# Kernel tuning notes

Measured on AMD Instinct MI355X. Metric: run time of the kernel, lower is better.

## Reference

```python
import jax, jax.numpy as jnp
import numpy as np

B, L, D, H = 4, 2048, 1024, 16
HD = D // H
NEG = -1e9  # stands in for -inf in masks; identical softmax result, grad-safe
EPS = 1e-5


def _layer_norm(x, g, b):
    mu = jnp.mean(x, axis=-1, keepdims=True)
    var = jnp.mean((x - mu) ** 2, axis=-1, keepdims=True)
    return (x - mu) * jax.lax.rsqrt(var + EPS) * g + b


def setup_inputs() -> dict:
    key = jax.random.key(0)
    ks = jax.random.split(key, 8)
    x = jax.random.normal(ks[0], (B, L, D), dtype=jnp.float32)
    # length-based padding: valid lengths in [L//2, L]; True = padded position
    lengths = jax.random.randint(ks[1], (B,), L // 2, L + 1)
    padding_mask = jnp.arange(L)[None, :] >= lengths[:, None]  # (B, L) bool
    # additive causal mask: 0 on/below diagonal, NEG above
    causal_mask = jnp.where(jnp.tril(jnp.ones((L, L), dtype=bool)), 0.0, NEG).astype(jnp.float32)

    def linear_params(k, fan_in, fan_out):
        bound = float(np.sqrt(6.0 / (fan_in + fan_out)))  # xavier_uniform
        W = jax.random.uniform(k, (fan_out, fan_in), jnp.float32, -bound, bound)
        b = jnp.zeros((fan_out,), jnp.float32)
        return W, b

    Wq, bq = linear_params(ks[2], D, D)
    Wk, bk = linear_params(ks[3], D, D)
    Wv, bv = linear_params(ks[4], D, D)
    Wo, bo = linear_params(ks[5], D, D)
    g_pre = jnp.ones((D,), jnp.float32); b_pre = jnp.zeros((D,), jnp.float32)
    g_ln = jnp.ones((D,), jnp.float32); b_ln = jnp.zeros((D,), jnp.float32)
    return {
        "x": x, "padding_mask": padding_mask, "causal_mask": causal_mask,
        "Wq": Wq, "bq": bq, "Wk": Wk, "bk": bk, "Wv": Wv, "bv": bv,
        "Wo": Wo, "bo": bo, "g_pre": g_pre, "b_pre": b_pre,
        "g_ln": g_ln, "b_ln": b_ln,
    }


def reference(x, padding_mask, causal_mask, Wq, bq, Wk, bk, Wv, bv, Wo, bo,
              g_pre, b_pre, g_ln, b_ln):
    # pre-LayerNorm (residual uses the normed x, matching the torch code)
    h = _layer_norm(x, g_pre, b_pre)  # (B, L, D)

    def heads(W, b):
        y = jnp.einsum('bld,ed->ble', h, W) + b           # torch Linear: x @ W.T + b
        return y.reshape(B, L, H, HD).transpose(0, 2, 1, 3)  # (B, H, L, HD)

    q, k, v = heads(Wq, bq), heads(Wk, bk), heads(Wv, bv)

    scores = jnp.einsum('bhld,bhmd->bhlm', q, k) / jnp.sqrt(jnp.float32(HD))
    scores = scores + causal_mask  # additive causal mask broadcast over (B, H)
    # padding mask: True = masked key position
    scores = jnp.where(padding_mask[:, None, None, :], NEG, scores)
    attn = jax.nn.softmax(scores, axis=-1)  # dropout p=0.0 (eval / disabled)

    out = jnp.einsum('bhlm,bhmd->bhld', attn, v)          # (B, H, L, HD)
    out = out.transpose(0, 2, 1, 3).reshape(B, L, D)
    out = jnp.einsum('bld,ed->ble', out, Wo) + bo
    return _layer_norm(out + h, g_ln, b_ln)
```

## Files before the change

kernel.cpp:

```cpp
#include <hip/hip_runtime.h>


#define Bq 4
#define Lq 2048
#define Dq 1024
#define Hq 16
#define HDq 64
#define Mq (Bq * Lq)

typedef __attribute__((ext_vector_type(8))) short short8;
typedef __attribute__((ext_vector_type(4))) float f32x4;
typedef __attribute__((address_space(3))) unsigned char lds_byte;
typedef __attribute__((address_space(1))) unsigned char gbl_byte;

__device__ __forceinline__ unsigned short f2b(float f) {
    unsigned int u = __float_as_uint(f);
    unsigned int r = (u + 0x7fffu + ((u >> 16) & 1u)) >> 16;
    return (unsigned short)r;
}
__device__ __forceinline__ float b2f(unsigned short u) {
    return __uint_as_float(((unsigned int)u) << 16);
}
__device__ __forceinline__ unsigned int packbf(float lo, float hi) {
    return (unsigned int)f2b(lo) | ((unsigned int)f2b(hi) << 16);
}

#define GLL16(gsrc, ldst)                                              \
    __builtin_amdgcn_global_load_lds((const gbl_byte*)(gsrc),          \
                                     (lds_byte*)(ldst), 16, 0, 0)

__global__ void setup_kernel(const unsigned char* __restrict__ m8,
                             int* __restrict__ lengths) {
    __shared__ int bad;
    __shared__ int fo[4];
    const int tid = threadIdx.x;
    if (tid == 0) bad = 0;
    if (tid < 4) fo[tid] = Lq;
    __syncthreads();
    for (int i = tid; i < Bq * Lq; i += 256) {
        unsigned char v = m8[i];
        if (v) {
            int r = i >> 11, c = i & (Lq - 1);
            atomicMin(&fo[r], c);
            if (c < Lq / 2) atomicOr(&bad, 1);
            else if (c < Lq - 1 && m8[i + 1] == 0) atomicOr(&bad, 1);
        }
    }
    __syncthreads();
    int anyone = (fo[0] < Lq) | (fo[1] < Lq) | (fo[2] < Lq) | (fo[3] < Lq);
    bool use8 = (bad == 0) && anyone;
    if (!use8) {
        __syncthreads();
        if (tid < 4) fo[tid] = Lq;
        __syncthreads();
        const int* m32 = (const int*)m8;
        for (int i = tid; i < Bq * Lq; i += 256) {
            if (m32[i] != 0) atomicMin(&fo[i >> 11], i & (Lq - 1));
        }
        __syncthreads();
    }
    if (tid < 4) lengths[tid] = fo[tid];
}

__global__ __launch_bounds__(256) void cvt4_kernel(
    const float* __restrict__ s0, const float* __restrict__ s1,
    const float* __restrict__ s2, const float* __restrict__ s3,
    unsigned short* __restrict__ dst) {
    const int region = blockIdx.x >> 10;
    const int i = (blockIdx.x & 1023) * 256 + threadIdx.x;
    const float* src = (region == 0) ? s0 : (region == 1) ? s1
                       : (region == 2) ? s2 : s3;
    float4 v = ((const float4*)src)[i];
    ushort4 o;
    o.x = f2b(v.x); o.y = f2b(v.y); o.z = f2b(v.z); o.w = f2b(v.w);
    ((ushort4*)dst)[(size_t)region * (Dq * Dq / 4) + i] = o;
}

__global__ __launch_bounds__(256) void ln_pre_kernel(
    const float* __restrict__ x, const float* __restrict__ g,
    const float* __restrict__ bb, unsigned short* __restrict__ out) {
    const int row = blockIdx.x, tid = threadIdx.x;
    float4 u = ((const float4*)x)[(size_t)row * 256 + tid];
    float s = u.x + u.y + u.z + u.w;
    float ss = u.x * u.x + u.y * u.y + u.z * u.z + u.w * u.w;
#pragma unroll
    for (int off = 32; off > 0; off >>= 1) {
        s += __shfl_xor(s, off);
        ss += __shfl_xor(ss, off);
    }
    __shared__ float sred[4], ssred[4];
    const int w = tid >> 6, lane = tid & 63;
    if (lane == 0) { sred[w] = s; ssred[w] = ss; }
    __syncthreads();
    s = sred[0] + sred[1] + sred[2] + sred[3];
    ss = ssred[0] + ssred[1] + ssred[2] + ssred[3];
    const float mean = s * (1.f / Dq);
    const float rstd = rsqrtf(ss * (1.f / Dq) - mean * mean + 1e-5f);
    float4 gv = ((const float4*)g)[tid];
    float4 bv = ((const float4*)bb)[tid];
    ushort4 o;
    o.x = f2b((u.x - mean) * rstd * gv.x + bv.x);
    o.y = f2b((u.y - mean) * rstd * gv.y + bv.y);
    o.z = f2b((u.z - mean) * rstd * gv.z + bv.z);
    o.w = f2b((u.w - mean) * rstd * gv.w + bv.w);
    ((ushort4*)out)[(size_t)row * 256 + tid] = o;
}

__global__ __launch_bounds__(256) void qkv_gemm_kernel(
    const unsigned short* __restrict__ A, const unsigned short* __restrict__ W3,
    const float* __restrict__ bq, const float* __restrict__ bk,
    const float* __restrict__ bv, unsigned short* __restrict__ Qo,
    unsigned short* __restrict__ Ko, unsigned short* __restrict__ Vto) {
    __shared__ unsigned short As[128][32];
    __shared__ unsigned short Bs[128][32];
    const int tid = threadIdx.x;
    const int w = tid >> 6, lane = tid & 63;
    const int lm = lane & 15, lq = lane >> 4;
    const int m0 = blockIdx.y << 7, n0 = blockIdx.x << 7;
    const int wm = (w >> 1) << 6, wn = (w & 1) << 6;
    f32x4 acc[4][4];
#pragma unroll
    for (int i = 0; i < 4; ++i)
#pragma unroll
        for (int j = 0; j < 4; ++j) acc[i][j] = (f32x4){0.f, 0.f, 0.f, 0.f};
    for (int k0 = 0; k0 < Dq; k0 += 32) {
        __syncthreads();
#pragma unroll
        for (int j = 0; j < 2; ++j) {
            const int base = j * 256 + w * 64;
            const int slot = base + lane;
            const int row = slot >> 2, c = slot & 3;
            GLL16(A + (size_t)(m0 + row) * Dq + k0 + c * 8,
                  (unsigned short*)As + base * 8);
            GLL16(W3 + (size_t)(n0 + row) * Dq + k0 + c * 8,
                  (unsigned short*)Bs + base * 8);
        }
        __syncthreads();
        short8 af[4], bf[4];
#pragma unroll
        for (int t = 0; t < 4; ++t)
            af[t] = *(const short8*)&As[wm + t * 16 + lm][lq * 8];
#pragma unroll
        for (int t = 0; t < 4; ++t)
            bf[t] = *(const short8*)&Bs[wn + t * 16 + lm][lq * 8];
#pragma unroll
        for (int mt = 0; mt < 4; ++mt)
#pragma unroll
            for (int nt = 0; nt < 4; ++nt)
                acc[mt][nt] = __builtin_amdgcn_mfma_f32_16x16x32_bf16(
                    af[mt], bf[nt], acc[mt][nt], 0, 0, 0);
    }
    const int region = n0 >> 10;
    const float* bias = (region == 0) ? bq : (region == 1) ? bk : bv;
    const float scale = (region == 0) ? 0.125f : 1.0f;
    const int nb = n0 & 1023;
#pragma unroll
    for (int nt = 0; nt < 4; ++nt) {
        const int colb = nb + wn + nt * 16 + lm;
        const float bval = bias[colb];
#pragma unroll
        for (int mt = 0; mt < 4; ++mt) {
            const int row0 = m0 + wm + mt * 16 + lq * 4;
            const int bidx = row0 >> 11, l0r = row0 & (Lq - 1);
            if (region < 2) {
                unsigned short* dst = (region == 0) ? Qo : Ko;
#pragma unroll
                for (int r = 0; r < 4; ++r)
                    dst[((size_t)(bidx * Hq + (colb >> 6)) * Lq + l0r + r) *
                            HDq + (colb & 63)] =
                        f2b((acc[mt][nt][r] + bval) * scale);
            } else {
                ushort4 o;
                o.x = f2b(acc[mt][nt][0] + bval);
                o.y = f2b(acc[mt][nt][1] + bval);
                o.z = f2b(acc[mt][nt][2] + bval);
                o.w = f2b(acc[mt][nt][3] + bval);
                *(ushort4*)&Vto[((size_t)(bidx * Hq + (colb >> 6)) * HDq +
                                 (colb & 63)) * Lq + l0r] = o;
            }
        }
    }
}

__global__ __launch_bounds__(256) void proj_gemm_kernel(
    const unsigned short* __restrict__ A, const unsigned short* __restrict__ Bw,
    const float* __restrict__ bias, float* __restrict__ Cout) {
    __shared__ unsigned short As[128][32];
    __shared__ unsigned short Bs[128][32];
    const int tid = threadIdx.x;
    const int w = tid >> 6, lane = tid & 63;
    const int lm = lane & 15, lq = lane >> 4;
    const int m0 = blockIdx.y << 7, n0 = blockIdx.x << 7;
    const int wm = (w >> 1) << 6, wn = (w & 1) << 6;
    f32x4 acc[4][4];
#pragma unroll
    for (int i = 0; i < 4; ++i)
#pragma unroll
        for (int j = 0; j < 4; ++j) acc[i][j] = (f32x4){0.f, 0.f, 0.f, 0.f};
    for (int k0 = 0; k0 < Dq; k0 += 32) {
        __syncthreads();
#pragma unroll
        for (int j = 0; j < 2; ++j) {
            const int base = j * 256 + w * 64;
            const int slot = base + lane;
            const int row = slot >> 2, c = slot & 3;
            const int rr = m0 + row, kk = k0 + c * 8;
            GLL16(A + ((size_t)((rr >> 11) * Hq + (kk >> 6)) * Lq +
                       (rr & (Lq - 1))) * HDq + (kk & 63),
                  (unsigned short*)As + base * 8);
            GLL16(Bw + (size_t)(n0 + row) * Dq + k0 + c * 8,
                  (unsigned short*)Bs + base * 8);
        }
        __syncthreads();
        short8 af[4], bf[4];
#pragma unroll
        for (int t = 0; t < 4; ++t)
            af[t] = *(const short8*)&As[wm + t * 16 + lm][lq * 8];
#pragma unroll
        for (int t = 0; t < 4; ++t)
            bf[t] = *(const short8*)&Bs[wn + t * 16 + lm][lq * 8];
#pragma unroll
        for (int mt = 0; mt < 4; ++mt)
#pragma unroll
            for (int nt = 0; nt < 4; ++nt)
                acc[mt][nt] = __builtin_amdgcn_mfma_f32_16x16x32_bf16(
                    af[mt], bf[nt], acc[mt][nt], 0, 0, 0);
    }
#pragma unroll
    for (int nt = 0; nt < 4; ++nt) {
        const float bval = bias[n0 + wn + nt * 16 + lm];
#pragma unroll
        for (int mt = 0; mt < 4; ++mt)
#pragma unroll
            for (int r = 0; r < 4; ++r)
                Cout[(size_t)(m0 + wm + mt * 16 + lq * 4 + r) * Dq + n0 + wn +
                     nt * 16 + lm] = acc[mt][nt][r] + bval;
    }
}

__global__ __launch_bounds__(256) void attn_kernel(
    const unsigned short* __restrict__ Qg, const unsigned short* __restrict__ Kg,
    const unsigned short* __restrict__ Vtg, const int* __restrict__ lengths,
    unsigned short* __restrict__ Og) {
    __shared__ unsigned short Ps[4][16][72];
    const int bx = blockIdx.x;
    const int hh = blockIdx.y, b = blockIdx.z;
    const int tid = threadIdx.x, w = tid >> 6, lane = tid & 63;
    const int lm = lane & 15, lq = lane >> 4;
    const int len = lengths[b];
    const int mxk = (len + 63) >> 6;
    const size_t hb = (size_t)(b * Hq + hh) * Lq * HDq;
    const unsigned short* Vb = Vtg + hb;

#pragma unroll
    for (int pass = 0; pass < 2; ++pass) {
        const int qt = pass ? bx : (15 - bx);
        const int l0 = qt << 7;
        short8 qf[2][2];
#pragma unroll
        for (int s = 0; s < 2; ++s)
#pragma unroll
            for (int h = 0; h < 2; ++h)
                qf[s][h] = *(const short8*)(Qg + hb +
                    (size_t)(l0 + w * 32 + s * 16 + lm) * HDq + h * 32 + lq * 8);
        f32x4 oacc[2][4];
        float m_i[2], l_i[2];
#pragma unroll
        for (int s = 0; s < 2; ++s) {
            m_i[s] = -1e30f; l_i[s] = 0.f;
#pragma unroll
            for (int t = 0; t < 4; ++t)
                oacc[s][t] = (f32x4){0.f, 0.f, 0.f, 0.f};
        }
        int nkt = 2 * qt + 2;
        if (nkt > mxk) nkt = mxk;
        for (int kt = 0; kt < nkt; ++kt) {
            const int kb = kt << 6;
            short8 kf[4][2], vf[4][2];
#pragma unroll
            for (int t = 0; t < 4; ++t)
#pragma unroll
                for (int h = 0; h < 2; ++h)
                    kf[t][h] = *(const short8*)(Kg + hb +
                        (size_t)(kb + t * 16 + lm) * HDq + h * 32 + lq * 8);
#pragma unroll
            for (int t = 0; t < 4; ++t)
#pragma unroll
                for (int kh = 0; kh < 2; ++kh)
                    vf[t][kh] = *(const short8*)(Vb +
                        (size_t)(t * 16 + lm) * Lq + kb + kh * 32 + lq * 8);
#pragma unroll
            for (int s = 0; s < 2; ++s) {
                f32x4 sc[4];
#pragma unroll
                for (int t = 0; t < 4; ++t) {
                    f32x4 z = (f32x4){0.f, 0.f, 0.f, 0.f};
                    z = __builtin_amdgcn_mfma_f32_16x16x32_bf16(
                        kf[t][0], qf[s][0], z, 0, 0, 0);
                    z = __builtin_amdgcn_mfma_f32_16x16x32_bf16(
                        kf[t][1], qf[s][1], z, 0, 0, 0);
                    sc[t] = z;
                }
                const int qmin = l0 + w * 32 + s * 16;
                float pvv[16];
                float mx = -1e30f;
                if ((kb + 63 <= qmin) && (kb + 63 < len)) {
#pragma unroll
                    for (int i = 0; i < 16; ++i) {
                        const float v = sc[i >> 2][i & 3];
                        pvv[i] = v;
                        mx = fmaxf(mx, v);
                    }
                } else {
                    const int q = qmin + lm;
#pragma unroll
                    for (int t = 0; t < 4; ++t)
#pragma unroll
                        for (int r = 0; r < 4; ++r) {
                            const int key = kb + t * 16 + lq * 4 + r;
                            float v = sc[t][r];
                            if (key > q || key >= len) v = -1e30f;
                            pvv[t * 4 + r] = v;
                            mx = fmaxf(mx, v);
                        }
                }
                mx = fmaxf(mx, __shfl_xor(mx, 16));
                mx = fmaxf(mx, __shfl_xor(mx, 32));
                const float mnew = fmaxf(m_i[s], mx);
                const float alpha = __expf(m_i[s] - mnew);
                m_i[s] = mnew;
                float psum = 0.f;
#pragma unroll
                for (int i = 0; i < 16; ++i) {
                    const float p = __expf(pvv[i] - mnew);
                    pvv[i] = p;
                    psum += p;
                }
                psum += __shfl_xor(psum, 16);
                psum += __shfl_xor(psum, 32);
                l_i[s] = l_i[s] * alpha + psum;
#pragma unroll
                for (int t = 0; t < 4; ++t) {
                    oacc[s][t][0] *= alpha; oacc[s][t][1] *= alpha;
                    oacc[s][t][2] *= alpha; oacc[s][t][3] *= alpha;
                }
#pragma unroll
                for (int t = 0; t < 4; ++t) {
                    uint2 uu;
                    uu.x = packbf(pvv[t * 4 + 0], pvv[t * 4 + 1]);
                    uu.y = packbf(pvv[t * 4 + 2], pvv[t * 4 + 3]);
                    *(uint2*)&Ps[w][lm][t * 16 + lq * 4] = uu;
                }
                asm volatile("s_waitcnt lgkmcnt(0)" ::: "memory");
                short8 pf0 = *(const short8*)&Ps[w][lm][lq * 8];
                short8 pf1 = *(const short8*)&Ps[w][lm][32 + lq * 8];
#pragma unroll
                for (int t = 0; t < 4; ++t) {
                    oacc[s][t] = __builtin_amdgcn_mfma_f32_16x16x32_bf16(
                        vf[t][0], pf0, oacc[s][t], 0, 0, 0);
                    oacc[s][t] = __builtin_amdgcn_mfma_f32_16x16x32_bf16(
                        vf[t][1], pf1, oacc[s][t], 0, 0, 0);
                }
            }
        }
#pragma unroll
        for (int s = 0; s < 2; ++s) {
            const float inv = 1.f / l_i[s];
            unsigned short* Ot =
                Og + hb + (size_t)(l0 + w * 32 + s * 16 + lm) * HDq;
#pragma unroll
            for (int t = 0; t < 4; ++t) {
                ushort4 o;
                o.x = f2b(oacc[s][t][0] * inv);
                o.y = f2b(oacc[s][t][1] * inv);
                o.z = f2b(oacc[s][t][2] * inv);
                o.w = f2b(oacc[s][t][3] * inv);
                *(ushort4*)(Ot + t * 16 + lq * 4) = o;
            }
        }
    }
}

__global__ __launch_bounds__(256) void ln_final_kernel(
    const float* __restrict__ pj, const unsigned short* __restrict__ h,
    const float* __restrict__ g, const float* __restrict__ bb,
    float* __restrict__ out) {
    const int row = blockIdx.x, tid = threadIdx.x;
    float4 a = ((const float4*)pj)[(size_t)row * 256 + tid];
    ushort4 hv = ((const ushort4*)h)[(size_t)row * 256 + tid];
    float f0 = a.x + b2f(hv.x), f1 = a.y + b2f(hv.y);
    float f2 = a.z + b2f(hv.z), f3 = a.w + b2f(hv.w);
    float s = f0 + f1 + f2 + f3;
    float ss = f0 * f0 + f1 * f1 + f2 * f2 + f3 * f3;
#pragma unroll
    for (int off = 32; off > 0; off >>= 1) {
        s += __shfl_xor(s, off);
        ss += __shfl_xor(ss, off);
    }
    __shared__ float sred[4], ssred[4];
    const int w = tid >> 6, lane = tid & 63;
    if (lane == 0) { sred[w] = s; ssred[w] = ss; }
    __syncthreads();
    s = sred[0] + sred[1] + sred[2] + sred[3];
    ss = ssred[0] + ssred[1] + ssred[2] + ssred[3];
    const float mean = s * (1.f / Dq);
    const float rstd = rsqrtf(ss * (1.f / Dq) - mean * mean + 1e-5f);
    float4 gv = ((const float4*)g)[tid];
    float4 bv = ((const float4*)bb)[tid];
    float4 o;
    o.x = (f0 - mean) * rstd * gv.x + bv.x;
    o.y = (f1 - mean) * rstd * gv.y + bv.y;
    o.z = (f2 - mean) * rstd * gv.z + bv.z;
    o.w = (f3 - mean) * rstd * gv.w + bv.w;
    ((float4*)out)[(size_t)row * 256 + tid] = o;
}

extern "C" void kernel_launch(void* const* d_in, const int* in_sizes, int n_in,
                              void* d_out, int out_size, void* d_ws,
                              size_t ws_size, hipStream_t stream) {
    const float* x = (const float*)d_in[0];
    const unsigned char* mask = (const unsigned char*)d_in[1];
    const float* Wq = (const float*)d_in[3];
    const float* bq = (const float*)d_in[4];
    const float* Wk = (const float*)d_in[5];
    const float* bk = (const float*)d_in[6];
    const float* Wv = (const float*)d_in[7];
    const float* bvv = (const float*)d_in[8];
    const float* Wo = (const float*)d_in[9];
    const float* bo = (const float*)d_in[10];
    const float* g_pre = (const float*)d_in[11];
    const float* b_pre = (const float*)d_in[12];
    const float* g_ln = (const float*)d_in[13];
    const float* b_ln = (const float*)d_in[14];

    const size_t SZ = (size_t)Mq * Dq;
    const size_t WSZ = (size_t)Dq * Dq;
    unsigned short* h = (unsigned short*)d_ws;
    unsigned short* q = h + SZ;
    unsigned short* k = q + SZ;
    unsigned short* vT = k + SZ;
    unsigned short* at = vT + SZ;
    unsigned short* W3 = at + SZ;
    unsigned short* wob = W3 + 3 * WSZ;
    float* proj = (float*)(wob + WSZ);
    int* lengths = (int*)(proj + SZ);

    setup_kernel<<<1, 256, 0, stream>>>(mask, lengths);
    cvt4_kernel<<<4096, 256, 0, stream>>>(Wq, Wk, Wv, Wo, W3);
    ln_pre_kernel<<<Mq, 256, 0, stream>>>(x, g_pre, b_pre, h);

    qkv_gemm_kernel<<<dim3(3 * Dq / 128, Mq / 128), 256, 0, stream>>>(
        h, W3, bq, bk, bvv, q, k, vT);
    attn_kernel<<<dim3(Lq / 256, Hq, Bq), 256, 0, stream>>>(q, k, vT, lengths,
                                                            at);
    proj_gemm_kernel<<<dim3(Dq / 128, Mq / 128), 256, 0, stream>>>(at, wob, bo,
                                                                   proj);
    ln_final_kernel<<<Mq, 256, 0, stream>>>(proj, h, g_ln, b_ln,
                                            (float*)d_out);
}
```

Before: 408.6 us.

## Double-buffer K/V tiles in LDS for attention and swizzle GEMM block order

The attention kernel now stages K and V tiles into XOR-swizzled LDS double buffers with async global-to-LDS loads. The next tile is prefetched while the current one is computed, replacing per-wave direct global loads. It also splits the QK MFMA phase from the softmax/PV phase, adds s_setprio around MFMA bursts, and sets occupancy launch bounds. Separately, the QKV and output projection GEMMs remap block indices for better L2 locality. The cost is more LDS per block and one extra barrier per key tile.

```diff
diff --git a/kernel.cpp b/kernel.cpp
--- a/kernel.cpp
+++ b/kernel.cpp
@@ -28,6 +28,9 @@
 #define GLL16(gsrc, ldst)                                              \
     __builtin_amdgcn_global_load_lds((const gbl_byte*)(gsrc),          \
                                      (lds_byte*)(ldst), 16, 0, 0)
+
+#define MFMA_BF16(A, B, C) \
+    __builtin_amdgcn_mfma_f32_16x16x32_bf16((A), (B), (C), 0, 0, 0)
 
 __global__ void setup_kernel(const unsigned char* __restrict__ m8,
                              int* __restrict__ lengths) {
@@ -116,7 +119,9 @@
     const int tid = threadIdx.x;
     const int w = tid >> 6, lane = tid & 63;
     const int lm = lane & 15, lq = lane >> 4;
-    const int m0 = blockIdx.y << 7, n0 = blockIdx.x << 7;
+    const int lin = blockIdx.y * 24 + blockIdx.x;
+    const int swz = (lin & 7) * (1536 / 8) + (lin >> 3);
+    const int m0 = (swz / 24) << 7, n0 = (swz % 24) << 7;
     const int wm = (w >> 1) << 6, wn = (w & 1) << 6;
     f32x4 acc[4][4];
 #pragma unroll
@@ -190,7 +195,9 @@
     const int tid = threadIdx.x;
     const int w = tid >> 6, lane = tid & 63;
     const int lm = lane & 15, lq = lane >> 4;
-    const int m0 = blockIdx.y << 7, n0 = blockIdx.x << 7;
+    const int lin = blockIdx.y * 8 + blockIdx.x;
+    const int swz = (lin & 7) * (512 / 8) + (lin >> 3);
+    const int m0 = (swz >> 3) << 7, n0 = (swz & 7) << 7;
     const int wm = (w >> 1) << 6, wn = (w & 1) << 6;
     f32x4 acc[4][4];
 #pragma unroll
@@ -238,11 +245,13 @@
     }
 }
 
-__global__ __launch_bounds__(256) void attn_kernel(
+__global__ __launch_bounds__(256, 2) void attn_kernel(
     const unsigned short* __restrict__ Qg, const unsigned short* __restrict__ Kg,
     const unsigned short* __restrict__ Vtg, const int* __restrict__ lengths,
     unsigned short* __restrict__ Og) {
-    __shared__ unsigned short Ps[4][16][72];
+    __shared__ unsigned short Kbuf[2][4096];
+    __shared__ unsigned short Vbuf[2][4096];
+    __shared__ unsigned short Ps[4][2][16][72];
     const int bx = blockIdx.x;
     const int hh = blockIdx.y, b = blockIdx.z;
     const int tid = threadIdx.x, w = tid >> 6, lane = tid & 63;
@@ -252,6 +261,21 @@
     const size_t hb = (size_t)(b * Hq + hh) * Lq * HDq;
     const unsigned short* Vb = Vtg + hb;
 
+    const int srow = w * 8 + (lane >> 3);
+    const int ssw = (lane & 7) ^ (lane >> 3);
+    const unsigned short* pK = Kg + hb + (size_t)srow * HDq + ssw * 8;
+    const unsigned short* pV = Vb + (size_t)srow * Lq + ssw * 8;
+
+#define STAGE_KV(BUF, KB)                                                   \
+    {                                                                       \
+        GLL16(pK + (size_t)(KB)*HDq, &Kbuf[(BUF)][(w * 64) * 8]);           \
+        GLL16(pK + (size_t)((KB) + 32) * HDq,                               \
+              &Kbuf[(BUF)][(256 + w * 64) * 8]);                            \
+        GLL16(pV + (KB), &Vbuf[(BUF)][(w * 64) * 8]);                       \
+        GLL16(pV + (size_t)32 * Lq + (KB),                                  \
+              &Vbuf[(BUF)][(256 + w * 64) * 8]);                            \
+    }
+
 #pragma unroll
     for (int pass = 0; pass < 2; ++pass) {
         const int qt = pass ? bx : (15 - bx);
@@ -274,52 +298,58 @@
         }
         int nkt = 2 * qt + 2;
         if (nkt > mxk) nkt = mxk;
+        STAGE_KV(0, 0);
+        __syncthreads();
         for (int kt = 0; kt < nkt; ++kt) {
             const int kb = kt << 6;
+            const int cur = kt & 1;
+            if (kt + 1 < nkt) STAGE_KV(cur ^ 1, (kt + 1) << 6);
             short8 kf[4][2], vf[4][2];
 #pragma unroll
-            for (int t = 0; t < 4; ++t)
-#pragma unroll
-                for (int h = 0; h < 2; ++h)
-                    kf[t][h] = *(const short8*)(Kg + hb +
-                        (size_t)(kb + t * 16 + lm) * HDq + h * 32 + lq * 8);
-#pragma unroll
-            for (int t = 0; t < 4; ++t)
-#pragma unroll
-                for (int kh = 0; kh < 2; ++kh)
-                    vf[t][kh] = *(const short8*)(Vb +
-                        (size_t)(t * 16 + lm) * Lq + kb + kh * 32 + lq * 8);
+            for (int t = 0; t < 4; ++t) {
+                const int ro = (t * 16 + lm) * 64;
+                const int sx = lm & 7;
+#pragma unroll
+                for (int h = 0; h < 2; ++h) {
+                    const int off = ro + (((h * 4 + lq) ^ sx) << 3);
+                    kf[t][h] = *(const short8*)&Kbuf[cur][off];
+                    vf[t][h] = *(const short8*)&Vbuf[cur][off];
+                }
+            }
+            f32x4 sc[2][4];
+            __builtin_amdgcn_s_setprio(1);
 #pragma unroll
             for (int s = 0; s < 2; ++s) {
-                f32x4 sc[4];
 #pragma unroll
                 for (int t = 0; t < 4; ++t) {
                     f32x4 z = (f32x4){0.f, 0.f, 0.f, 0.f};
-                    z = __builtin_amdgcn_mfma_f32_16x16x32_bf16(
-                        kf[t][0], qf[s][0], z, 0, 0, 0);
-                    z = __builtin_amdgcn_mfma_f32_16x16x32_bf16(
-                        kf[t][1], qf[s][1], z, 0, 0, 0);
-                    sc[t] = z;
-                }
+                    z = MFMA_BF16(kf[t][0], qf[s][0], z);
+                    z = MFMA_BF16(kf[t][1], qf[s][1], z);
+                    sc[s][t] = z;
+                }
+            }
+            __builtin_amdgcn_s_setprio(0);
+#pragma unroll
+            for (int s = 0; s < 2; ++s) {
                 const int qmin = l0 + w * 32 + s * 16;
                 float pvv[16];
                 float mx = -1e30f;
                 if ((kb + 63 <= qmin) && (kb + 63 < len)) {
 #pragma unroll
                     for (int i = 0; i < 16; ++i) {
-                        const float v = sc[i >> 2][i & 3];
+                        const float v = sc[s][i >> 2][i & 3];
                         pvv[i] = v;
                         mx = fmaxf(mx, v);
                     }
                 } else {
-                    const int q = qmin + lm;
+                    const int qq = qmin + lm;
 #pragma unroll
                     for (int t = 0; t < 4; ++t)
 #pragma unroll
                         for (int r = 0; r < 4; ++r) {
                             const int key = kb + t * 16 + lq * 4 + r;
-                            float v = sc[t][r];
-                            if (key > q || key >= len) v = -1e30f;
+                            float v = sc[s][t][r];
+                            if (key > qq || key >= len) v = -1e30f;
                             pvv[t * 4 + r] = v;
                             mx = fmaxf(mx, v);
                         }
@@ -327,8 +357,6 @@
                 mx = fmaxf(mx, __shfl_xor(mx, 16));
                 mx = fmaxf(mx, __shfl_xor(mx, 32));
                 const float mnew = fmaxf(m_i[s], mx);
-                const float alpha = __expf(m_i[s] - mnew);
-                m_i[s] = mnew;
                 float psum = 0.f;
 #pragma unroll
                 for (int i = 0; i < 16; ++i) {
@@ -336,32 +364,38 @@
                     pvv[i] = p;
                     psum += p;
                 }
-                psum += __shfl_xor(psum, 16);
-                psum += __shfl_xor(psum, 32);
-                l_i[s] = l_i[s] * alpha + psum;
-#pragma unroll
-                for (int t = 0; t < 4; ++t) {
-                    oacc[s][t][0] *= alpha; oacc[s][t][1] *= alpha;
-                    oacc[s][t][2] *= alpha; oacc[s][t][3] *= alpha;
-                }
 #pragma unroll
                 for (int t = 0; t < 4; ++t) {
                     uint2 uu;
                     uu.x = packbf(pvv[t * 4 + 0], pvv[t * 4 + 1]);
                     uu.y = packbf(pvv[t * 4 + 2], pvv[t * 4 + 3]);
-                    *(uint2*)&Ps[w][lm][t * 16 + lq * 4] = uu;
-                }
-                asm volatile("s_waitcnt lgkmcnt(0)" ::: "memory");
-                short8 pf0 = *(const short8*)&Ps[w][lm][lq * 8];
-                short8 pf1 = *(const short8*)&Ps[w][lm][32 + lq * 8];
+                    *(uint2*)&Ps[w][s][lm][t * 16 + lq * 4] = uu;
+                }
+                psum += __shfl_xor(psum, 16);
+                psum += __shfl_xor(psum, 32);
+                const float alpha = __expf(m_i[s] - mnew);
+                m_i[s] = mnew;
+                l_i[s] = l_i[s] * alpha + psum;
 #pragma unroll
                 for (int t = 0; t < 4; ++t) {
-                    oacc[s][t] = __builtin_amdgcn_mfma_f32_16x16x32_bf16(
-                        vf[t][0], pf0, oacc[s][t], 0, 0, 0);
-                    oacc[s][t] = __builtin_amdgcn_mfma_f32_16x16x32_bf16(
-                        vf[t][1], pf1, oacc[s][t], 0, 0, 0);
-                }
-            }
+                    oacc[s][t][0] *= alpha; oacc[s][t][1] *= alpha;
+                    oacc[s][t][2] *= alpha; oacc[s][t][3] *= alpha;
+                }
+            }
+            asm volatile("s_waitcnt lgkmcnt(0)" ::: "memory");
+            __builtin_amdgcn_s_setprio(1);
+#pragma unroll
+            for (int s = 0; s < 2; ++s) {
+                short8 pf0 = *(const short8*)&Ps[w][s][lm][lq * 8];
+                short8 pf1 = *(const short8*)&Ps[w][s][lm][32 + lq * 8];
+#pragma unroll
+                for (int t = 0; t < 4; ++t) {
+                    oacc[s][t] = MFMA_BF16(vf[t][0], pf0, oacc[s][t]);
+                    oacc[s][t] = MFMA_BF16(vf[t][1], pf1, oacc[s][t]);
+                }
+            }
+            __builtin_amdgcn_s_setprio(0);
+            __syncthreads();
         }
 #pragma unroll
         for (int s = 0; s < 2; ++s) {
@@ -379,6 +413,7 @@
             }
         }
     }
+#undef STAGE_KV
 }
 
 __global__ __launch_bounds__(256) void ln_final_kernel(
```

Result: faster. 360.7 us (-11.7%).
